# Kernel optimization log

Measured on AMD Instinct MI355X. Metric: run time of the kernel, lower is better.

Reference implementation:

```python
import jax, jax.numpy as jnp
import numpy as np

THR = 10.0           # spike threshold (all layers, igarss2023 config)
LEAK1, LEAK2, LEAK3 = 9.0, 1.0, 0.0  # subtractive leak per layer
POOL1_K, POOL1_S = 7, 6
POOL2_K, POOL2_S = 2, 2
WTA_BLOCK = 2        # local spatial WTA window


def conv2d_same(x, w):
    # x: (B,C,H,W), w: (O,I,kh,kw)
    return jax.lax.conv_general_dilated(
        x, w, window_strides=(1, 1), padding='SAME',
        dimension_numbers=('NCHW', 'OIHW', 'NCHW'))


def maxpool(x, k, s):
    return jax.lax.reduce_window(
        x, -jnp.inf, jax.lax.max, (1, 1, k, k), (1, 1, s, s), 'VALID')


def wta(mem, spk, block=WTA_BLOCK):
    """Winner-take-all lateral inhibition ('both' mode):
    (1) channel competition: only the channel with max membrane at each
        spatial location may spike; (2) local spatial competition: only the
        max-membrane neuron within each block x block window of each map
        may spike. Requires H,W divisible by block."""
    C = mem.shape[1]
    ch_win = jnp.argmax(mem, axis=1)                         # (B,H,W)
    ch_mask = jax.nn.one_hot(ch_win, C, axis=1, dtype=mem.dtype)  # (B,C,H,W)
    loc = jax.lax.reduce_window(
        mem, -jnp.inf, jax.lax.max,
        (1, 1, block, block), (1, 1, block, block), 'VALID')
    loc_up = jnp.repeat(jnp.repeat(loc, block, axis=2), block, axis=3)
    sp_mask = (mem >= loc_up).astype(mem.dtype)
    return spk * ch_mask * sp_mask


def lif_step(mem, inp, leak, use_wta):
    # integrate -> threshold -> WTA -> reset-to-zero -> subtractive leak
    mem = mem + inp
    spk = (mem >= THR).astype(mem.dtype)
    if use_wta:
        spk = wta(mem, spk)
    mem = jnp.where(spk > 0, 0.0, mem)
    mem = jnp.maximum(mem - leak, 0.0)
    return mem, spk


def setup_inputs() -> dict:
    key = jax.random.key(0)
    k0, k1, k2, k3 = jax.random.split(key, 4)
    T, B, H, W = 20, 8, 256, 256
    x = jax.random.uniform(k0, (T, B, 1, H, W), dtype=jnp.float32)
    # STDP-style weights are non-negative in [0,1)
    w1 = jax.random.uniform(k1, (4, 1, 5, 5), dtype=jnp.float32)
    w2 = jax.random.uniform(k2, (36, 4, 5, 5), dtype=jnp.float32)
    w3 = jax.random.uniform(k3, (1, 36, 7, 7), dtype=jnp.float32)
    return {"x": x, "w1": w1, "w2": w2, "w3": w3}


def reference(x, w1, w2, w3):
    T, B, _, H, W = x.shape
    H1, W1 = H, W                                   # conv1 SAME
    H2 = (H1 - POOL1_K) // POOL1_S + 1              # 42
    W2 = (W1 - POOL1_K) // POOL1_S + 1
    H3 = (H2 - POOL2_K) // POOL2_S + 1              # 21
    W3 = (W2 - POOL2_K) // POOL2_S + 1
    C1, C2, C3 = w1.shape[0], w2.shape[0], w3.shape[0]

    m1_0 = jnp.zeros((B, C1, H1, W1), x.dtype)
    m2_0 = jnp.zeros((B, C2, H2, W2), x.dtype)
    m3_0 = jnp.zeros((B, C3, H3, W3), x.dtype)

    def step(carry, xt):
        m1, m2, m3 = carry
        m1, s1 = lif_step(m1, conv2d_same(xt, w1), LEAK1, True)
        p1 = maxpool(s1, POOL1_K, POOL1_S)
        m2, s2 = lif_step(m2, conv2d_same(p1, w2), LEAK2, True)
        p2 = maxpool(s2, POOL2_K, POOL2_S)
        m3, s3 = lif_step(m3, conv2d_same(p2, w3), LEAK3, False)
        return (m1, m2, m3), s3

    _, cls_spikes = jax.lax.scan(step, (m1_0, m2_0, m3_0), x)
    return cls_spikes  # (T, B, n_classes, H3, W3)
```

## Files before the change

kernel.cpp:

```cpp
#include <hip/hip_runtime.h>
#include <stdint.h>

#define THR 10.0f
#define AGT __HIP_MEMORY_SCOPE_AGENT

static constexpr size_t OFF_P2  = 1048576;
static constexpr size_t OFF_BAR = 1245184;

static __device__ __forceinline__ uint32_t ldu32(const uint32_t* p) {
    return __hip_atomic_load(p, __ATOMIC_RELAXED, AGT);
}
static __device__ __forceinline__ void stu32(uint32_t* p, uint32_t v) {
    __hip_atomic_store(p, v, __ATOMIC_RELAXED, AGT);
}
static __device__ __forceinline__ void stu16(uint16_t* p, uint16_t v) {
    __hip_atomic_store(p, v, __ATOMIC_RELAXED, AGT);
}
static __device__ __forceinline__ uint32_t rmwread(uint32_t* p) {
    return __hip_atomic_fetch_add(p, 0u, __ATOMIC_RELAXED, AGT);
}

__global__ __launch_bounds__(256) void zero_bar(uint32_t* __restrict__ bar) {
    if (threadIdx.x < 256) bar[threadIdx.x] = 0u;
}

__device__ __forceinline__ void gbar(uint32_t* bar, int bid, uint32_t n) {
    __syncthreads();
    if (threadIdx.x == 0) {
        uint32_t* base = bar + (bid >> 6) * 32;
        uint32_t a = __hip_atomic_fetch_add(base, 1u, __ATOMIC_RELAXED, AGT);
        if (a == 64u * n - 1u)
            __hip_atomic_fetch_add(base + 16, 1u, __ATOMIC_RELAXED, AGT);
        while (rmwread(base + 16) < n)
            __builtin_amdgcn_s_sleep(2);
    }
    __syncthreads();
}

__global__ __launch_bounds__(256, 2) void spike_persist(
    const float* __restrict__ x,
    const float* __restrict__ w1,
    const float* __restrict__ w2,
    const float* __restrict__ w3,
    float* __restrict__ out,
    uint8_t* __restrict__ s1b,
    uint8_t* __restrict__ p2b,
    uint32_t* __restrict__ bar)
{
    __shared__ union {
        float    xs[2112];
        uint32_t st32[527];
    } u;
    __shared__ float    ps[400];
    __shared__ float    mem_s[1296];
    __shared__ float    bm_s[324];
    __shared__ int      wc_s[36];
    __shared__ uint32_t p2a[18];

    const int tid = threadIdx.x;
    const int bid = blockIdx.x;
    uint32_t nbar = 0;

    const int b1 = bid >> 6;
    const int r0 = (bid & 63) * 4;
    const int tr = tid >> 7, tc = tid & 127;
    const int py = r0 + 2 * tr;
    const int px = 2 * tc;

    const int tIdx = bid & 63;
    const int b2 = bid >> 6;
    const int tyi = tIdx >> 3, txi = tIdx & 7;
    const int oy2 = tyi < 5 ? 6 * tyi : 30 + 4 * (tyi - 5);
    const int ox2 = txi < 5 ? 6 * txi : 30 + 4 * (txi - 5);
    const int th2 = tyi < 5 ? 6 : 4;
    const int tw2 = txi < 5 ? 6 : 4;
    const int wave = tid >> 6, lane = tid & 63;
    const int pr = lane / 6, pc = lane - 6 * pr;
    const bool act = (pr < th2) && (pc < tw2);
    const int prA = pr > 5 ? 0 : pr, pcA = pc;

    const int lid3 = (bid & 63) * 4 + wave;
    const int kyl = lane / 7, kxl = lane % 7;

    float w3v[36];
#pragma unroll
    for (int c = 0; c < 36; c++) w3v[c] = (lane < 49) ? w3[c * 49 + lane] : 0.f;

    float m1r[4][2][2];
#pragma unroll
    for (int c = 0; c < 4; c++)
#pragma unroll
        for (int dy = 0; dy < 2; dy++)
#pragma unroll
            for (int dx = 0; dx < 2; dx++) m1r[c][dy][dx] = 0.f;
    float m2r[9];
#pragma unroll
    for (int i = 0; i < 9; i++) m2r[i] = 0.f;
    float m3r[2] = {0.f, 0.f};

    for (int k = 0; k < 12; k++) {
        for (int tt = 0; tt < 2; tt++) {
            const int t = 2 * k + tt;
            if (t >= 20) break;
            uint16_t* s1w = reinterpret_cast<uint16_t*>(s1b + (size_t)(t & 3) * 262144);
            const float* xb = x + ((size_t)t * 8 + b1) * 65536;
            __syncthreads();
#pragma unroll
            for (int i = 0; i < 9; i++) {
                int idx = tid + i * 256;
                if (idx < 2112) {
                    int row = idx / 264, col = idx - row * 264;
                    int gy = r0 + row - 2, gx = col - 2;
                    float v = 0.f;
                    if (gy >= 0 && gy < 256 && gx >= 0 && gx < 256) v = xb[gy * 256 + gx];
                    u.xs[idx] = v;
                }
            }
            __syncthreads();

            float p[6][6];
#pragma unroll
            for (int i = 0; i < 6; i++)
#pragma unroll
                for (int j = 0; j < 6; j++)
                    p[i][j] = u.xs[(2 * tr + i) * 264 + 2 * tc + j];

            float acc[4][2][2];
#pragma unroll
            for (int c = 0; c < 4; c++)
#pragma unroll
                for (int dy = 0; dy < 2; dy++)
#pragma unroll
                    for (int dx = 0; dx < 2; dx++) acc[c][dy][dx] = 0.f;
#pragma unroll
            for (int c = 0; c < 4; c++)
#pragma unroll
                for (int ky = 0; ky < 5; ky++)
#pragma unroll
                    for (int kx = 0; kx < 5; kx++) {
                        float w = w1[c * 25 + ky * 5 + kx];
#pragma unroll
                        for (int dy = 0; dy < 2; dy++)
#pragma unroll
                            for (int dx = 0; dx < 2; dx++)
                                acc[c][dy][dx] = fmaf(p[dy + ky][dx + kx], w, acc[c][dy][dx]);
                    }

            float mem[4][2][2];
#pragma unroll
            for (int c = 0; c < 4; c++)
#pragma unroll
                for (int dy = 0; dy < 2; dy++)
#pragma unroll
                    for (int dx = 0; dx < 2; dx++)
                        mem[c][dy][dx] = m1r[c][dy][dx] + acc[c][dy][dx];

            int wc[2][2];
#pragma unroll
            for (int dy = 0; dy < 2; dy++)
#pragma unroll
                for (int dx = 0; dx < 2; dx++) {
                    int w = 0; float mx = mem[0][dy][dx];
#pragma unroll
                    for (int c = 1; c < 4; c++) {
                        float v = mem[c][dy][dx];
                        if (v > mx) { mx = v; w = c; }
                    }
                    wc[dy][dx] = w;
                }

            float bm[4];
#pragma unroll
            for (int c = 0; c < 4; c++)
                bm[c] = fmaxf(fmaxf(mem[c][0][0], mem[c][0][1]), fmaxf(mem[c][1][0], mem[c][1][1]));

            uint32_t bits = 0;
#pragma unroll
            for (int c = 0; c < 4; c++)
#pragma unroll
                for (int dy = 0; dy < 2; dy++)
#pragma unroll
                    for (int dx = 0; dx < 2; dx++) {
                        float m = mem[c][dy][dx];
                        bool s = (m >= THR) && (wc[dy][dx] == c) && (m >= bm[c]);
                        m1r[c][dy][dx] = fmaxf((s ? 0.f : m) - 9.0f, 0.f);
                        bits |= (s ? 1u : 0u) << (c * 4 + dy * 2 + dx);
                    }
            stu16(s1w + ((size_t)(b1 * 128 + (r0 >> 1) + tr)) * 128 + tc, (uint16_t)bits);
        }

        for (int tt = 0; tt < 2; tt++) {
            const int tl = 2 * k - 4 + tt;
            if (tl < 0 || tl >= 20) continue;
            const uint32_t* pb32 = reinterpret_cast<const uint32_t*>(
                p2b + (size_t)(tl % 6) * 32768);
#pragma unroll
            for (int rep = 0; rep < 2; rep++) {
                int o = lid3 + rep * 256;
                if (o < 441) {
                    int rr = o / 21, cl = o - rr * 21;
                    int yy = rr + kyl - 3, xx = cl + kxl - 3;
                    bool inb = (lane < 49) && yy >= 0 && yy < 21 && xx >= 0 && xx < 21;
                    uint32_t lo = 0, hi = 0;
                    if (inb) {
                        const uint32_t* pc = pb32 + (((size_t)b2 * 441 + yy * 21 + xx) << 1);
                        lo = ldu32(pc);
                        hi = ldu32(pc + 1);
                    }
                    float accv = 0.f;
#pragma unroll
                    for (int c = 0; c < 32; c++) accv += ((lo >> c) & 1u) ? w3v[c] : 0.f;
#pragma unroll
                    for (int c = 0; c < 4; c++)  accv += ((hi >> c) & 1u) ? w3v[32 + c] : 0.f;
#pragma unroll
                    for (int off = 32; off; off >>= 1) accv += __shfl_xor(accv, off, 64);
                    float memv3 = m3r[rep] + accv;
                    bool s = memv3 >= THR;
                    if (lane == 0) out[(size_t)tl * 3528 + b2 * 441 + o] = s ? 1.f : 0.f;
                    m3r[rep] = fmaxf(s ? 0.f : memv3, 0.f);
                }
            }
        }

        for (int tt = 0; tt < 2; tt++) {
            const int tb = 2 * k - 2 + tt;
            if (tb < 0 || tb >= 20) continue;
            const uint32_t* s1r32 = reinterpret_cast<const uint32_t*>(
                s1b + (size_t)(tb & 3) * 262144);
            uint32_t* p2w32 = reinterpret_cast<uint32_t*>(p2b + (size_t)(tb % 6) * 32768);

            const int rb0 = 3 * oy2 - 6;
            const int cb0 = (3 * ox2 - 6) >> 1;

            __syncthreads();
#pragma unroll
            for (int i = 0; i < 3; i++) {
                int idx = tid + i * 256;
                if (idx < 527) {
                    int row = idx / 17, w = idx - row * 17;
                    int grow = rb0 + row, gcol = cb0 + w;
                    uint32_t v = 0;
                    if (grow >= 0 && grow < 128 && gcol >= 0 && gcol < 64)
                        v = ldu32(s1r32 + ((size_t)b2 * 128 + grow) * 64 + gcol);
                    u.st32[idx] = v;
                }
            }
            __syncthreads();

            if (tid < 100) {
                int r = tid / 10, cc2 = tid - 10 * r;
                int gy = oy2 - 2 + r, gx = ox2 - 2 + cc2;
                uint32_t accb = 0;
                if (r < th2 + 4 && cc2 < tw2 + 4 && gy >= 0 && gy < 42 && gx >= 0 && gx < 42) {
                    const uint16_t* st16 = reinterpret_cast<const uint16_t*>(u.st32);
#pragma unroll
                    for (int kr = 0; kr < 4; kr++)
#pragma unroll
                        for (int kc = 0; kc < 4; kc++) {
                            uint32_t m = (kr < 3) ? (kc < 3 ? 0xFu : 0x5u)
                                                  : (kc < 3 ? 0x3u : 0x1u);
                            uint32_t v = st16[(3 * r + kr) * 34 + 3 * cc2 + kc];
                            accb |= v & (m * 0x1111u);
                        }
                }
#pragma unroll
                for (int ic = 0; ic < 4; ic++)
                    ps[ic * 100 + tid] = ((accb >> (4 * ic)) & 0xFu) ? 1.f : 0.f;
            }
            __syncthreads();

            float pv[4][5][5];
#pragma unroll
            for (int ic = 0; ic < 4; ic++)
#pragma unroll
                for (int i = 0; i < 5; i++)
#pragma unroll
                    for (int j = 0; j < 5; j++)
                        pv[ic][i][j] = ps[ic * 100 + (prA + i) * 10 + (pcA + j)];

            float memv[9];
            for (int cc = 0; cc < 9; cc++) {
                int c = cc * 4 + wave;
                const float* wr = w2 + (size_t)__builtin_amdgcn_readfirstlane(c) * 100;
                float accv = 0.f;
#pragma unroll
                for (int ic = 0; ic < 4; ic++)
#pragma unroll
                    for (int i = 0; i < 5; i++)
#pragma unroll
                        for (int j = 0; j < 5; j++)
                            accv = fmaf(pv[ic][i][j], wr[ic * 25 + i * 5 + j], accv);
                float m = act ? (m2r[cc] + accv) : -1e30f;
                memv[cc] = m;
                if (lane < 36) mem_s[c * 36 + lane] = m;
            }
            __syncthreads();

            if (tid < 36) {
                float mx = mem_s[tid]; int w = 0;
#pragma unroll
                for (int c = 1; c < 36; c++) {
                    float v = mem_s[c * 36 + tid];
                    if (v > mx) { mx = v; w = c; }
                }
                wc_s[tid] = w;
            }
#pragma unroll
            for (int i = 0; i < 2; i++) {
                int idx = tid + i * 256;
                if (idx < 324) {
                    int c = idx / 9, blk = idx - 9 * c;
                    int br = blk / 3, bc2 = blk - 3 * br;
                    int l0 = 12 * br + 2 * bc2;
                    float a = mem_s[c * 36 + l0],     bb2 = mem_s[c * 36 + l0 + 1];
                    float d = mem_s[c * 36 + l0 + 6], e   = mem_s[c * 36 + l0 + 7];
                    bm_s[idx] = fmaxf(fmaxf(a, bb2), fmaxf(d, e));
                }
            }
            if (tid < 18) p2a[tid] = 0;
            __syncthreads();

            const int blkl = (pr >> 1) * 3 + (pc >> 1);
            for (int cc = 0; cc < 9; cc++) {
                int c = cc * 4 + wave;
                if (act) {
                    float m = memv[cc];
                    bool s = (m >= THR) && (wc_s[lane] == c) && (m >= bm_s[c * 9 + blkl]);
                    m2r[cc] = fmaxf((s ? 0.f : m) - 1.0f, 0.f);
                }
            }

#pragma unroll
            for (int i = 0; i < 2; i++) {
                int idx = tid + i * 256;
                if (idx < 324) {
                    int c = idx / 9, blk = idx - 9 * c;
                    int br = blk / 3, bc2 = blk - 3 * br;
                    if (2 * br < th2 && 2 * bc2 < tw2) {
                        int l0 = 12 * br + 2 * bc2;
                        float bmv = bm_s[idx];
                        bool any = false;
#pragma unroll
                        for (int kk = 0; kk < 4; kk++) {
                            int l = l0 + (kk >> 1) * 6 + (kk & 1);
                            float m = mem_s[c * 36 + l];
                            any |= (m >= THR) && (wc_s[l] == c) && (m >= bmv);
                        }
                        if (any)
                            atomicOr(&p2a[(blk << 1) + (c >> 5)], 1u << (c & 31));
                    }
                }
            }
            __syncthreads();

            if (tid < 9) {
                int br = tid / 3, bc2 = tid - 3 * br;
                if (2 * br < th2 && 2 * bc2 < tw2) {
                    int cell = b2 * 441 + ((oy2 >> 1) + br) * 21 + (ox2 >> 1) + bc2;
                    uint32_t* dst = p2w32 + ((size_t)cell << 1);
                    stu32(dst, p2a[tid * 2]);
                    stu32(dst + 1, p2a[tid * 2 + 1]);
                }
            }
        }

        if (k < 11) gbar(bar, bid, ++nbar);
    }
}

extern "C" void kernel_launch(void* const* d_in, const int* in_sizes, int n_in,
                              void* d_out, int out_size, void* d_ws, size_t ws_size,
                              hipStream_t stream) {
    const float* x  = (const float*)d_in[0];
    const float* w1 = (const float*)d_in[1];
    const float* w2 = (const float*)d_in[2];
    const float* w3 = (const float*)d_in[3];
    float* out = (float*)d_out;
    uint8_t* s1 = (uint8_t*)d_ws;
    uint8_t* p2 = (uint8_t*)d_ws + OFF_P2;
    uint32_t* bar = (uint32_t*)((char*)d_ws + OFF_BAR);

    zero_bar<<<1, 256, 0, stream>>>(bar);

    void* args[] = {(void*)&x, (void*)&w1, (void*)&w2, (void*)&w3,
                    (void*)&out, (void*)&s1, (void*)&p2, (void*)&bar};
    hipLaunchCooperativeKernel((void*)spike_persist, dim3(512), dim3(256),
                               args, 0, stream);
}
```

Baseline: 459.1 us.

## Double grid to 1024 blocks with 4 timesteps per barrier phase

```diff
diff --git a/kernel.cpp b/kernel.cpp
--- a/kernel.cpp
+++ b/kernel.cpp
@@ -4,8 +4,8 @@
 #define THR 10.0f
 #define AGT __HIP_MEMORY_SCOPE_AGENT
 
-static constexpr size_t OFF_P2  = 1048576;
-static constexpr size_t OFF_BAR = 1245184;
+static constexpr size_t OFF_P2  = 2097152;
+static constexpr size_t OFF_BAR = 2359296;
 
 static __device__ __forceinline__ uint32_t ldu32(const uint32_t* p) {
     return __hip_atomic_load(p, __ATOMIC_RELAXED, AGT);
@@ -27,9 +27,9 @@
 __device__ __forceinline__ void gbar(uint32_t* bar, int bid, uint32_t n) {
     __syncthreads();
     if (threadIdx.x == 0) {
-        uint32_t* base = bar + (bid >> 6) * 32;
+        uint32_t* base = bar + (bid >> 7) * 32;
         uint32_t a = __hip_atomic_fetch_add(base, 1u, __ATOMIC_RELAXED, AGT);
-        if (a == 64u * n - 1u)
+        if (a == 128u * n - 1u)
             __hip_atomic_fetch_add(base + 16, 1u, __ATOMIC_RELAXED, AGT);
         while (rmwread(base + 16) < n)
             __builtin_amdgcn_s_sleep(2);
@@ -37,7 +37,7 @@
     __syncthreads();
 }
 
-__global__ __launch_bounds__(256, 2) void spike_persist(
+__global__ __launch_bounds__(256, 4) void spike_persist(
     const float* __restrict__ x,
     const float* __restrict__ w1,
     const float* __restrict__ w2,
@@ -48,323 +48,297 @@
     uint32_t* __restrict__ bar)
 {
     __shared__ union {
-        float    xs[2112];
-        uint32_t st32[527];
+        float    xs[1560];
+        uint32_t st32[403];
     } u;
-    __shared__ float    ps[400];
-    __shared__ float    mem_s[1296];
-    __shared__ float    bm_s[324];
-    __shared__ int      wc_s[36];
-    __shared__ uint32_t p2a[18];
+    __shared__ float    ps[320];
+    __shared__ float    mem_s[864];
+    __shared__ float    w3s[1764];
+    __shared__ uint32_t p2a[12];
 
     const int tid = threadIdx.x;
     const int bid = blockIdx.x;
     uint32_t nbar = 0;
 
-    const int b1 = bid >> 6;
-    const int r0 = (bid & 63) * 4;
-    const int tr = tid >> 7, tc = tid & 127;
-    const int py = r0 + 2 * tr;
-    const int px = 2 * tc;
-
-    const int tIdx = bid & 63;
-    const int b2 = bid >> 6;
-    const int tyi = tIdx >> 3, txi = tIdx & 7;
+    const int b1 = bid >> 7;
+    const int strip = bid & 127;
+    const int r0 = strip * 2;
+
+    const int tIdx = bid & 127;
+    const int b2 = bid >> 7;
+    const int tyi = tIdx >> 4, txi = tIdx & 15;
     const int oy2 = tyi < 5 ? 6 * tyi : 30 + 4 * (tyi - 5);
-    const int ox2 = txi < 5 ? 6 * txi : 30 + 4 * (txi - 5);
+    const int ox2 = txi < 5 ? 4 * txi : 20 + 2 * (txi - 5);
     const int th2 = tyi < 5 ? 6 : 4;
-    const int tw2 = txi < 5 ? 6 : 4;
+    const int tw2 = txi < 5 ? 4 : 2;
     const int wave = tid >> 6, lane = tid & 63;
-    const int pr = lane / 6, pc = lane - 6 * pr;
+    const int pr = lane >> 2, pc = lane & 3;
     const bool act = (pr < th2) && (pc < tw2);
-    const int prA = pr > 5 ? 0 : pr, pcA = pc;
-
-    const int lid3 = (bid & 63) * 4 + wave;
+    const int prA = act ? pr : 0, pcA = act ? pc : 0;
+    const bool rep = act && !(pr & 1) && !(pc & 1);
+    const int blkl = (pr >> 1) * 2 + (pc >> 1);
+
+    const int wid3 = (bid & 127) * 4 + wave;
+    const bool o441 = wid3 < 441;
     const int kyl = lane / 7, kxl = lane % 7;
-
-    float w3v[36];
-#pragma unroll
-    for (int c = 0; c < 36; c++) w3v[c] = (lane < 49) ? w3[c * 49 + lane] : 0.f;
-
-    float m1r[4][2][2];
-#pragma unroll
-    for (int c = 0; c < 4; c++)
-#pragma unroll
-        for (int dy = 0; dy < 2; dy++)
-#pragma unroll
-            for (int dx = 0; dx < 2; dx++) m1r[c][dy][dx] = 0.f;
+    bool l3v; int l3o;
+    {
+        int rr = wid3 / 21, cl = wid3 - rr * 21;
+        int yy = rr + kyl - 3, xx = cl + kxl - 3;
+        l3v = o441 && (lane < 49) && yy >= 0 && yy < 21 && xx >= 0 && xx < 21;
+        l3o = (b2 * 441 + yy * 21 + xx) << 1;
+    }
+
+    int aoff[7]; bool aval[7];
+#pragma unroll
+    for (int i = 0; i < 7; i++) {
+        int idx = tid + i * 256;
+        int row = idx / 260, col = idx - row * 260;
+        int gy = r0 + row - 2, gx = col - 2;
+        aval[i] = (idx < 1560) && gy >= 0 && gy < 256 && gx >= 0 && gx < 256;
+        aoff[i] = gy * 256 + gx;
+    }
+    const int s1soff = (b1 * 128 + strip) * 128 + (tid >> 1);
+
+    const int rb0 = 3 * oy2 - 6;
+    const int cb0 = (3 * ox2 - 6) >> 1;
+    int boff[2]; bool bval[2];
+#pragma unroll
+    for (int i = 0; i < 2; i++) {
+        int idx = tid + i * 256;
+        int row = idx / 13, w = idx - row * 13;
+        int grow = rb0 + row, gcol = cb0 + w;
+        bval[i] = (idx < 403) && grow >= 0 && grow < 128 && gcol >= 0 && gcol < 64;
+        boff[i] = (b2 * 128 + grow) * 64 + gcol;
+    }
+
+#pragma unroll
+    for (int i = 0; i < 7; i++) {
+        int idx = tid + i * 256;
+        if (idx < 1764) w3s[idx] = w3[idx];
+    }
+
+    float m1r[4][2];
+#pragma unroll
+    for (int c = 0; c < 4; c++) { m1r[c][0] = 0.f; m1r[c][1] = 0.f; }
     float m2r[9];
 #pragma unroll
     for (int i = 0; i < 9; i++) m2r[i] = 0.f;
-    float m3r[2] = {0.f, 0.f};
-
-    for (int k = 0; k < 12; k++) {
-        for (int tt = 0; tt < 2; tt++) {
-            const int t = 2 * k + tt;
-            if (t >= 20) break;
-            uint16_t* s1w = reinterpret_cast<uint16_t*>(s1b + (size_t)(t & 3) * 262144);
-            const float* xb = x + ((size_t)t * 8 + b1) * 65536;
-            __syncthreads();
-#pragma unroll
-            for (int i = 0; i < 9; i++) {
-                int idx = tid + i * 256;
-                if (idx < 2112) {
-                    int row = idx / 264, col = idx - row * 264;
-                    int gy = r0 + row - 2, gx = col - 2;
-                    float v = 0.f;
-                    if (gy >= 0 && gy < 256 && gx >= 0 && gx < 256) v = xb[gy * 256 + gx];
-                    u.xs[idx] = v;
-                }
-            }
-            __syncthreads();
-
-            float p[6][6];
-#pragma unroll
-            for (int i = 0; i < 6; i++)
-#pragma unroll
-                for (int j = 0; j < 6; j++)
-                    p[i][j] = u.xs[(2 * tr + i) * 264 + 2 * tc + j];
-
-            float acc[4][2][2];
-#pragma unroll
-            for (int c = 0; c < 4; c++)
-#pragma unroll
-                for (int dy = 0; dy < 2; dy++)
-#pragma unroll
-                    for (int dx = 0; dx < 2; dx++) acc[c][dy][dx] = 0.f;
-#pragma unroll
-            for (int c = 0; c < 4; c++)
-#pragma unroll
-                for (int ky = 0; ky < 5; ky++)
-#pragma unroll
-                    for (int kx = 0; kx < 5; kx++) {
-                        float w = w1[c * 25 + ky * 5 + kx];
-#pragma unroll
-                        for (int dy = 0; dy < 2; dy++)
-#pragma unroll
-                            for (int dx = 0; dx < 2; dx++)
-                                acc[c][dy][dx] = fmaf(p[dy + ky][dx + kx], w, acc[c][dy][dx]);
-                    }
-
-            float mem[4][2][2];
-#pragma unroll
-            for (int c = 0; c < 4; c++)
-#pragma unroll
-                for (int dy = 0; dy < 2; dy++)
-#pragma unroll
-                    for (int dx = 0; dx < 2; dx++)
-                        mem[c][dy][dx] = m1r[c][dy][dx] + acc[c][dy][dx];
-
-            int wc[2][2];
-#pragma unroll
-            for (int dy = 0; dy < 2; dy++)
-#pragma unroll
-                for (int dx = 0; dx < 2; dx++) {
-                    int w = 0; float mx = mem[0][dy][dx];
+    float m3r = 0.f;
+
+    for (int k = 0; k < 7; k++) {
+        for (int tt = 0; tt < 4; tt++) {
+            const int t = 4 * k + tt;
+            if (t < 20) {
+                uint16_t* s1w = reinterpret_cast<uint16_t*>(s1b + (size_t)(t & 7) * 262144);
+                const float* xb = x + ((size_t)t * 8 + b1) * 65536;
+                __syncthreads();
+#pragma unroll
+                for (int i = 0; i < 7; i++) {
+                    int idx = tid + i * 256;
+                    if (idx < 1560) u.xs[idx] = aval[i] ? xb[aoff[i]] : 0.f;
+                }
+                __syncthreads();
+
+                float p[6][5];
+#pragma unroll
+                for (int i = 0; i < 6; i++)
+#pragma unroll
+                    for (int j = 0; j < 5; j++)
+                        p[i][j] = u.xs[i * 260 + tid + j];
+
+                float acc[4][2];
+#pragma unroll
+                for (int c = 0; c < 4; c++) { acc[c][0] = 0.f; acc[c][1] = 0.f; }
+#pragma unroll
+                for (int c = 0; c < 4; c++)
+#pragma unroll
+                    for (int ky = 0; ky < 5; ky++)
+#pragma unroll
+                        for (int kx = 0; kx < 5; kx++) {
+                            float w = w1[c * 25 + ky * 5 + kx];
+                            acc[c][0] = fmaf(p[ky][kx], w, acc[c][0]);
+                            acc[c][1] = fmaf(p[ky + 1][kx], w, acc[c][1]);
+                        }
+
+                float mem[4][2];
+#pragma unroll
+                for (int c = 0; c < 4; c++) {
+                    mem[c][0] = m1r[c][0] + acc[c][0];
+                    mem[c][1] = m1r[c][1] + acc[c][1];
+                }
+
+                int wc[2];
+#pragma unroll
+                for (int dy = 0; dy < 2; dy++) {
+                    int w = 0; float mx = mem[0][dy];
 #pragma unroll
                     for (int c = 1; c < 4; c++) {
-                        float v = mem[c][dy][dx];
+                        float v = mem[c][dy];
                         if (v > mx) { mx = v; w = c; }
                     }
-                    wc[dy][dx] = w;
-                }
-
-            float bm[4];
-#pragma unroll
-            for (int c = 0; c < 4; c++)
-                bm[c] = fmaxf(fmaxf(mem[c][0][0], mem[c][0][1]), fmaxf(mem[c][1][0], mem[c][1][1]));
-
-            uint32_t bits = 0;
-#pragma unroll
-            for (int c = 0; c < 4; c++)
-#pragma unroll
-                for (int dy = 0; dy < 2; dy++)
-#pragma unroll
-                    for (int dx = 0; dx < 2; dx++) {
-                        float m = mem[c][dy][dx];
-                        bool s = (m >= THR) && (wc[dy][dx] == c) && (m >= bm[c]);
-                        m1r[c][dy][dx] = fmaxf((s ? 0.f : m) - 9.0f, 0.f);
+                    wc[dy] = w;
+                }
+
+                float bm[4];
+#pragma unroll
+                for (int c = 0; c < 4; c++) {
+                    float own2 = fmaxf(mem[c][0], mem[c][1]);
+                    bm[c] = fmaxf(own2, __shfl_xor(own2, 1, 64));
+                }
+
+                uint32_t bits = 0;
+                const int dx = tid & 1;
+#pragma unroll
+                for (int c = 0; c < 4; c++)
+#pragma unroll
+                    for (int dy = 0; dy < 2; dy++) {
+                        float m = mem[c][dy];
+                        bool s = (m >= THR) && (wc[dy] == c) && (m >= bm[c]);
+                        m1r[c][dy] = fmaxf((s ? 0.f : m) - 9.0f, 0.f);
                         bits |= (s ? 1u : 0u) << (c * 4 + dy * 2 + dx);
                     }
-            stu16(s1w + ((size_t)(b1 * 128 + (r0 >> 1) + tr)) * 128 + tc, (uint16_t)bits);
-        }
-
-        for (int tt = 0; tt < 2; tt++) {
-            const int tl = 2 * k - 4 + tt;
-            if (tl < 0 || tl >= 20) continue;
-            const uint32_t* pb32 = reinterpret_cast<const uint32_t*>(
-                p2b + (size_t)(tl % 6) * 32768);
-#pragma unroll
-            for (int rep = 0; rep < 2; rep++) {
-                int o = lid3 + rep * 256;
-                if (o < 441) {
-                    int rr = o / 21, cl = o - rr * 21;
-                    int yy = rr + kyl - 3, xx = cl + kxl - 3;
-                    bool inb = (lane < 49) && yy >= 0 && yy < 21 && xx >= 0 && xx < 21;
-                    uint32_t lo = 0, hi = 0;
-                    if (inb) {
-                        const uint32_t* pc = pb32 + (((size_t)b2 * 441 + yy * 21 + xx) << 1);
-                        lo = ldu32(pc);
-                        hi = ldu32(pc + 1);
-                    }
-                    float accv = 0.f;
-#pragma unroll
-                    for (int c = 0; c < 32; c++) accv += ((lo >> c) & 1u) ? w3v[c] : 0.f;
-#pragma unroll
-                    for (int c = 0; c < 4; c++)  accv += ((hi >> c) & 1u) ? w3v[32 + c] : 0.f;
-#pragma unroll
-                    for (int off = 32; off; off >>= 1) accv += __shfl_xor(accv, off, 64);
-                    float memv3 = m3r[rep] + accv;
-                    bool s = memv3 >= THR;
-                    if (lane == 0) out[(size_t)tl * 3528 + b2 * 441 + o] = s ? 1.f : 0.f;
-                    m3r[rep] = fmaxf(s ? 0.f : memv3, 0.f);
-                }
+                bits |= (uint32_t)__shfl_xor((int)bits, 1, 64);
+                if (!(tid & 1)) stu16(s1w + s1soff, (uint16_t)bits);
             }
         }
 
-        for (int tt = 0; tt < 2; tt++) {
-            const int tb = 2 * k - 2 + tt;
-            if (tb < 0 || tb >= 20) continue;
-            const uint32_t* s1r32 = reinterpret_cast<const uint32_t*>(
-                s1b + (size_t)(tb & 3) * 262144);
-            uint32_t* p2w32 = reinterpret_cast<uint32_t*>(p2b + (size_t)(tb % 6) * 32768);
-
-            const int rb0 = 3 * oy2 - 6;
-            const int cb0 = (3 * ox2 - 6) >> 1;
-
-            __syncthreads();
-#pragma unroll
-            for (int i = 0; i < 3; i++) {
-                int idx = tid + i * 256;
-                if (idx < 527) {
-                    int row = idx / 17, w = idx - row * 17;
-                    int grow = rb0 + row, gcol = cb0 + w;
-                    uint32_t v = 0;
-                    if (grow >= 0 && grow < 128 && gcol >= 0 && gcol < 64)
-                        v = ldu32(s1r32 + ((size_t)b2 * 128 + grow) * 64 + gcol);
-                    u.st32[idx] = v;
-                }
-            }
-            __syncthreads();
-
-            if (tid < 100) {
-                int r = tid / 10, cc2 = tid - 10 * r;
-                int gy = oy2 - 2 + r, gx = ox2 - 2 + cc2;
-                uint32_t accb = 0;
-                if (r < th2 + 4 && cc2 < tw2 + 4 && gy >= 0 && gy < 42 && gx >= 0 && gx < 42) {
-                    const uint16_t* st16 = reinterpret_cast<const uint16_t*>(u.st32);
-#pragma unroll
-                    for (int kr = 0; kr < 4; kr++)
-#pragma unroll
-                        for (int kc = 0; kc < 4; kc++) {
-                            uint32_t m = (kr < 3) ? (kc < 3 ? 0xFu : 0x5u)
-                                                  : (kc < 3 ? 0x3u : 0x1u);
-                            uint32_t v = st16[(3 * r + kr) * 34 + 3 * cc2 + kc];
-                            accb |= v & (m * 0x1111u);
-                        }
-                }
-#pragma unroll
-                for (int ic = 0; ic < 4; ic++)
-                    ps[ic * 100 + tid] = ((accb >> (4 * ic)) & 0xFu) ? 1.f : 0.f;
-            }
-            __syncthreads();
-
-            float pv[4][5][5];
-#pragma unroll
-            for (int ic = 0; ic < 4; ic++)
-#pragma unroll
-                for (int i = 0; i < 5; i++)
-#pragma unroll
-                    for (int j = 0; j < 5; j++)
-                        pv[ic][i][j] = ps[ic * 100 + (prA + i) * 10 + (pcA + j)];
-
-            float memv[9];
-            for (int cc = 0; cc < 9; cc++) {
-                int c = cc * 4 + wave;
-                const float* wr = w2 + (size_t)__builtin_amdgcn_readfirstlane(c) * 100;
+        for (int tt = 0; tt < 4; tt++) {
+            const int tl = 4 * k - 8 + tt;
+            if (tl >= 0 && tl < 20 && o441) {
+                const uint32_t* pb32 = reinterpret_cast<const uint32_t*>(
+                    p2b + (size_t)(tl & 7) * 32768);
+                uint32_t lo = 0, hi = 0;
+                if (l3v) { lo = ldu32(pb32 + l3o); hi = ldu32(pb32 + l3o + 1); }
                 float accv = 0.f;
 #pragma unroll
-                for (int ic = 0; ic < 4; ic++)
-#pragma unroll
-                    for (int i = 0; i < 5; i++)
-#pragma unroll
-                        for (int j = 0; j < 5; j++)
-                            accv = fmaf(pv[ic][i][j], wr[ic * 25 + i * 5 + j], accv);
-                float m = act ? (m2r[cc] + accv) : -1e30f;
-                memv[cc] = m;
-                if (lane < 36) mem_s[c * 36 + lane] = m;
-            }
-            __syncthreads();
-
-            if (tid < 36) {
-                float mx = mem_s[tid]; int w = 0;
-#pragma unroll
-                for (int c = 1; c < 36; c++) {
-                    float v = mem_s[c * 36 + tid];
-                    if (v > mx) { mx = v; w = c; }
-                }
-                wc_s[tid] = w;
-            }
-#pragma unroll
-            for (int i = 0; i < 2; i++) {
-                int idx = tid + i * 256;
-                if (idx < 324) {
-                    int c = idx / 9, blk = idx - 9 * c;
-                    int br = blk / 3, bc2 = blk - 3 * br;
-                    int l0 = 12 * br + 2 * bc2;
-                    float a = mem_s[c * 36 + l0],     bb2 = mem_s[c * 36 + l0 + 1];
-                    float d = mem_s[c * 36 + l0 + 6], e   = mem_s[c * 36 + l0 + 7];
-                    bm_s[idx] = fmaxf(fmaxf(a, bb2), fmaxf(d, e));
-                }
-            }
-            if (tid < 18) p2a[tid] = 0;
-            __syncthreads();
-
-            const int blkl = (pr >> 1) * 3 + (pc >> 1);
-            for (int cc = 0; cc < 9; cc++) {
-                int c = cc * 4 + wave;
-                if (act) {
-                    float m = memv[cc];
-                    bool s = (m >= THR) && (wc_s[lane] == c) && (m >= bm_s[c * 9 + blkl]);
-                    m2r[cc] = fmaxf((s ? 0.f : m) - 1.0f, 0.f);
-                }
-            }
-
-#pragma unroll
-            for (int i = 0; i < 2; i++) {
-                int idx = tid + i * 256;
-                if (idx < 324) {
-                    int c = idx / 9, blk = idx - 9 * c;
-                    int br = blk / 3, bc2 = blk - 3 * br;
-                    if (2 * br < th2 && 2 * bc2 < tw2) {
-                        int l0 = 12 * br + 2 * bc2;
-                        float bmv = bm_s[idx];
-                        bool any = false;
-#pragma unroll
-                        for (int kk = 0; kk < 4; kk++) {
-                            int l = l0 + (kk >> 1) * 6 + (kk & 1);
-                            float m = mem_s[c * 36 + l];
-                            any |= (m >= THR) && (wc_s[l] == c) && (m >= bmv);
-                        }
-                        if (any)
-                            atomicOr(&p2a[(blk << 1) + (c >> 5)], 1u << (c & 31));
-                    }
-                }
-            }
-            __syncthreads();
-
-            if (tid < 9) {
-                int br = tid / 3, bc2 = tid - 3 * br;
-                if (2 * br < th2 && 2 * bc2 < tw2) {
-                    int cell = b2 * 441 + ((oy2 >> 1) + br) * 21 + (ox2 >> 1) + bc2;
-                    uint32_t* dst = p2w32 + ((size_t)cell << 1);
-                    stu32(dst, p2a[tid * 2]);
-                    stu32(dst + 1, p2a[tid * 2 + 1]);
-                }
+                for (int c = 0; c < 32; c++)
+                    accv += ((lo >> c) & 1u) ? w3s[c * 49 + lane] : 0.f;
+#pragma unroll
+                for (int c = 0; c < 4; c++)
+                    accv += ((hi >> c) & 1u) ? w3s[(32 + c) * 49 + lane] : 0.f;
+#pragma unroll
+                for (int off = 32; off; off >>= 1) accv += __shfl_xor(accv, off, 64);
+                float memv3 = m3r + accv;
+                bool s = memv3 >= THR;
+                if (lane == 0) out[(size_t)tl * 3528 + b2 * 441 + wid3] = s ? 1.f : 0.f;
+                m3r = fmaxf(s ? 0.f : memv3, 0.f);
             }
         }
 
-        if (k < 11) gbar(bar, bid, ++nbar);
+        for (int tt = 0; tt < 4; tt++) {
+            const int tb = 4 * k - 4 + tt;
+            if (tb >= 0 && tb < 20) {
+                const uint32_t* s1r32 = reinterpret_cast<const uint32_t*>(
+                    s1b + (size_t)(tb & 7) * 262144);
+                uint32_t* p2w32 = reinterpret_cast<uint32_t*>(p2b + (size_t)(tb & 7) * 32768);
+
+                __syncthreads();
+#pragma unroll
+                for (int i = 0; i < 2; i++) {
+                    int idx = tid + i * 256;
+                    if (idx < 403) u.st32[idx] = bval[i] ? ldu32(s1r32 + boff[i]) : 0u;
+                }
+                if (tid < 12) p2a[tid] = 0;
+                __syncthreads();
+
+                if (tid < 80) {
+                    int r = tid >> 3, cc2 = tid & 7;
+                    int gy = oy2 - 2 + r, gx = ox2 - 2 + cc2;
+                    uint32_t accb = 0;
+                    if (r < th2 + 4 && cc2 < tw2 + 4 && gy >= 0 && gy < 42 && gx >= 0 && gx < 42) {
+                        const uint16_t* st16 = reinterpret_cast<const uint16_t*>(u.st32);
+#pragma unroll
+                        for (int kr = 0; kr < 4; kr++)
+#pragma unroll
+                            for (int kc = 0; kc < 4; kc++) {
+                                uint32_t m = (kr < 3) ? (kc < 3 ? 0xFu : 0x5u)
+                                                      : (kc < 3 ? 0x3u : 0x1u);
+                                uint32_t v = st16[(3 * r + kr) * 26 + 3 * cc2 + kc];
+                                accb |= v & (m * 0x1111u);
+                            }
+                    }
+#pragma unroll
+                    for (int ic = 0; ic < 4; ic++)
+                        ps[ic * 80 + tid] = ((accb >> (4 * ic)) & 0xFu) ? 1.f : 0.f;
+                }
+                __syncthreads();
+
+                float accv[9];
+#pragma unroll
+                for (int cc = 0; cc < 9; cc++) accv[cc] = 0.f;
+#pragma unroll
+                for (int ic = 0; ic < 4; ic++) {
+                    float pv[5][5];
+#pragma unroll
+                    for (int i = 0; i < 5; i++)
+#pragma unroll
+                        for (int j = 0; j < 5; j++)
+                            pv[i][j] = ps[ic * 80 + (prA + i) * 8 + (pcA + j)];
+                    for (int cc = 0; cc < 9; cc++) {
+                        int c = cc * 4 + wave;
+                        const float* wr = w2 +
+                            (size_t)__builtin_amdgcn_readfirstlane(c) * 100 + ic * 25;
+#pragma unroll
+                        for (int i = 0; i < 5; i++)
+#pragma unroll
+                            for (int j = 0; j < 5; j++)
+                                accv[cc] = fmaf(pv[i][j], wr[i * 5 + j], accv[cc]);
+                    }
+                }
+
+                float memv[9];
+#pragma unroll
+                for (int cc = 0; cc < 9; cc++) {
+                    int c = cc * 4 + wave;
+                    float m = act ? (m2r[cc] + accv[cc]) : -1e30f;
+                    memv[cc] = m;
+                    if (lane < 24) mem_s[c * 24 + lane] = m;
+                }
+                __syncthreads();
+
+                int wcp = 0;
+                if (act) {
+                    float mx = mem_s[lane];
+#pragma unroll
+                    for (int c = 1; c < 36; c++) {
+                        float v = mem_s[c * 24 + lane];
+                        if (v > mx) { mx = v; wcp = c; }
+                    }
+                }
+                uint32_t oLo = 0, oHi = 0;
+#pragma unroll
+                for (int cc = 0; cc < 9; cc++) {
+                    int c = cc * 4 + wave;
+                    float m = memv[cc];
+                    float v1 = fmaxf(m, __shfl_xor(m, 1, 64));
+                    float bm = fmaxf(v1, __shfl_xor(v1, 4, 64));
+                    bool s = act && (m >= THR) && (wcp == c) && (m >= bm);
+                    if (act) m2r[cc] = fmaxf((s ? 0.f : m) - 1.0f, 0.f);
+                    uint32_t sv = s ? 1u : 0u;
+                    sv |= (uint32_t)__shfl_xor((int)sv, 1, 64);
+                    sv |= (uint32_t)__shfl_xor((int)sv, 4, 64);
+                    if (sv) { if (c < 32) oLo |= 1u << c; else oHi |= 1u << (c - 32); }
+                }
+                if (rep) {
+                    if (oLo) atomicOr(&p2a[blkl * 2], oLo);
+                    if (oHi) atomicOr(&p2a[blkl * 2 + 1], oHi);
+                }
+                __syncthreads();
+
+                if (tid < 6) {
+                    int cbr = tid >> 1, cbc = tid & 1;
+                    if (2 * cbr < th2 && 2 * cbc < tw2) {
+                        int cell = b2 * 441 + ((oy2 >> 1) + cbr) * 21 + (ox2 >> 1) + cbc;
+                        uint32_t* dst = p2w32 + ((size_t)cell << 1);
+                        stu32(dst, p2a[tid * 2]);
+                        stu32(dst + 1, p2a[tid * 2 + 1]);
+                    }
+                }
+            }
+        }
+
+        if (k < 6) gbar(bar, bid, ++nbar);
     }
 }
 
@@ -384,6 +358,6 @@
 
     void* args[] = {(void*)&x, (void*)&w1, (void*)&w2, (void*)&w3,
                     (void*)&out, (void*)&s1, (void*)&p2, (void*)&bar};
-    hipLaunchCooperativeKernel((void*)spike_persist, dim3(512), dim3(256),
+    hipLaunchCooperativeKernel((void*)spike_persist, dim3(1024), dim3(256),
                                args, 0, stream);
 }
```

After: 1.109 ms. 142% more time.
